# Kernel optimization log

Hardware: AMD Instinct MI355X
Metric: run time of the kernel (lower is better)

Reference implementation:

```python
import jax, jax.numpy as jnp
import numpy as np

N = 20000; E = 320000; IN = 512; H = 4; C = 128; HC = H * C; SD = 2; SE = 128
NEG = 0.01      # nn.LeakyReLU default slope (post-norm activations)
ATT_NEG = 0.2   # GATv2 attention LeakyReLU slope


def _gatv2(x, wl, bl, wr, br, att, bias, src, dst, concat):
    # PyG GATv2Conv (eval mode, add_self_loops already applied to src/dst)
    n = x.shape[0]
    xl = (x @ wl.T + bl).reshape(n, H, C)   # source-side projection
    xr = (x @ wr.T + br).reshape(n, H, C)   # target-side projection
    e = jax.nn.leaky_relu(xl[src] + xr[dst], ATT_NEG)        # [Etot, H, C]
    logits = jnp.einsum('ehc,hc->eh', e, att)                # [Etot, H]
    m = jax.ops.segment_max(logits, dst, num_segments=n)     # segment softmax over dst
    ez = jnp.exp(logits - m[dst])
    denom = jax.ops.segment_sum(ez, dst, num_segments=n)
    alpha = ez / denom[dst]
    out = jax.ops.segment_sum(xl[src] * alpha[:, :, None], dst, num_segments=n)  # [n, H, C]
    out = out.reshape(n, HC) if concat else out.mean(axis=1)
    return out + bias, alpha


def _bn(x, g, b):
    # BatchNorm1d, training-mode batch statistics (biased variance), eps=1e-5
    mu = x.mean(0)
    v = x.var(0)
    return g * (x - mu) * jax.lax.rsqrt(v + 1e-5) + b


def setup_inputs() -> dict:
    key = jax.random.key(0)
    ks = jax.random.split(key, 20)
    p = lambda i, shape: jax.random.normal(ks[i], shape, jnp.float32) * 0.05
    return dict(
        x=jax.random.normal(ks[0], (N, IN), jnp.float32),
        edge_index=jax.random.randint(ks[1], (2, E), 0, N),
        spatial_coords=jax.random.uniform(ks[2], (N, SD), dtype=jnp.float32),
        w1_l=p(3, (HC, IN)), b1_l=jnp.zeros((HC,)), w1_r=p(4, (HC, IN)), b1_r=jnp.zeros((HC,)),
        att1=p(5, (H, C)), bias1=jnp.zeros((HC,)), bn1_g=jnp.ones((HC,)), bn1_b=jnp.zeros((HC,)),
        w2_l=p(6, (HC, HC)), b2_l=jnp.zeros((HC,)), w2_r=p(7, (HC, HC)), b2_r=jnp.zeros((HC,)),
        att2=p(8, (H, C)), bias2=jnp.zeros((HC,)), bn2_g=jnp.ones((HC,)), bn2_b=jnp.zeros((HC,)),
        w3_l=p(9, (HC, HC)), b3_l=jnp.zeros((HC,)), w3_r=p(10, (HC, HC)), b3_r=jnp.zeros((HC,)),
        att3=p(11, (H, C)), bias3=jnp.zeros((C,)), bn3_g=jnp.ones((C,)), bn3_b=jnp.zeros((C,)),
        sp_w1=p(12, (SE, SD)), sp_b1=jnp.zeros((SE,)),
        sp_w2=p(13, (C, SE)), sp_b2=jnp.zeros((C,)),
        mha_in_w=p(14, (3 * SE, SE)), mha_in_b=jnp.zeros((3 * SE,)),
        mha_out_w=p(15, (SE, SE)), mha_out_b=jnp.zeros((SE,)),
        gate_w=p(16, (1, 2 * C)), gate_b=jnp.zeros((1,)),
    )


def reference(x, edge_index, spatial_coords,
              w1_l, b1_l, w1_r, b1_r, att1, bias1, bn1_g, bn1_b,
              w2_l, b2_l, w2_r, b2_r, att2, bias2, bn2_g, bn2_b,
              w3_l, b3_l, w3_r, b3_r, att3, bias3, bn3_g, bn3_b,
              sp_w1, sp_b1, sp_w2, sp_b2,
              mha_in_w, mha_in_b, mha_out_w, mha_out_b,
              gate_w, gate_b):
    loop = jnp.arange(N)
    src = jnp.concatenate([edge_index[0], loop])  # add self loops (PyG default)
    dst = jnp.concatenate([edge_index[1], loop])

    h1, a1 = _gatv2(x, w1_l, b1_l, w1_r, b1_r, att1, bias1, src, dst, True)
    h1 = jax.nn.leaky_relu(_bn(h1, bn1_g, bn1_b), NEG)
    h2, a2 = _gatv2(h1, w2_l, b2_l, w2_r, b2_r, att2, bias2, src, dst, True)
    h2 = jax.nn.leaky_relu(_bn(h2, bn2_g, bn2_b), NEG)
    z, a3 = _gatv2(h2, w3_l, b3_l, w3_r, b3_r, att3, bias3, src, dst, False)
    z = jax.nn.leaky_relu(_bn(z, bn3_g, bn3_b), NEG)

    # spatial embedding MLP (Linear -> LeakyReLU -> Linear -> LeakyReLU)
    emb = jax.nn.leaky_relu(spatial_coords @ sp_w1.T + sp_b1, NEG)
    emb = jax.nn.leaky_relu(emb @ sp_w2.T + sp_b2, NEG)
    # MultiheadAttention over a length-1 sequence: softmax over a single key is 1,
    # so output = W_o (W_v e + b_v) + b_o
    wv = mha_in_w[2 * SE:]
    bv = mha_in_b[2 * SE:]
    sp = (emb @ wv.T + bv) @ mha_out_w.T + mha_out_b  # [N, C]

    gate = jax.nn.softmax(jnp.concatenate([z, sp], axis=-1) @ gate_w.T + gate_b, axis=-1)  # [N,1] (all ones: size-1 softmax, faithful to source)
    z = gate * z + (1.0 - gate) * sp
    return z, a1, a2, a3, gate
```

## Files before the change

### kernel.cpp

```cpp
#include <hip/hip_runtime.h>
#include <math.h>

#define NN 20000
#define EE 320000
#define ETOT 340000
#define DEGCAP 128

typedef __attribute__((ext_vector_type(8))) short short8;
typedef __attribute__((ext_vector_type(4))) float f32x4;

__device__ __forceinline__ float lrelu(float x, float s) { return fmaxf(x, s * x); }
__device__ __forceinline__ float bf2f(ushort u) {
    union { uint i; float f; } c;
    c.i = ((uint)u) << 16;
    return c.f;
}
__device__ __forceinline__ ushort f2bf(float f) {
    uint u = __float_as_uint(f);
    uint r = (u + 0x7FFFu + ((u >> 16) & 1u)) >> 16;
    return (ushort)r;
}
__device__ __forceinline__ void gload16(const ushort* g, const ushort* l) {
    __builtin_amdgcn_global_load_lds((const __attribute__((address_space(1))) void*)g,
                                     (__attribute__((address_space(3))) void*)l, 16, 0, 0);
}

__global__ __launch_bounds__(1024) void k_scan(const int* __restrict__ counts, int* __restrict__ rstart) {
    __shared__ int sm[1024];
    int t = threadIdx.x;
    const int CH = 20;
    int base = t * CH;
    int loc[CH];
    int s = 0;
#pragma unroll
    for (int j = 0; j < CH; ++j) {
        int idx = base + j;
        int v = (idx < NN) ? counts[idx] : 0;
        loc[j] = s;
        s += v;
    }
    sm[t] = s;
    __syncthreads();
    for (int o = 1; o < 1024; o <<= 1) {
        int v = (t >= o) ? sm[t - o] : 0;
        __syncthreads();
        if (t >= o) sm[t] += v;
        __syncthreads();
    }
    int off = sm[t] - s;
#pragma unroll
    for (int j = 0; j < CH; ++j) {
        int idx = base + j;
        if (idx < NN) rstart[idx] = off + loc[j];
    }
    if (t == 1023) rstart[NN] = sm[1023];
}

__global__ void k_scatter(const int* __restrict__ ei, const int* __restrict__ rstart,
                          int* __restrict__ cursor, int* __restrict__ csr) {
    int i = blockIdx.x * blockDim.x + threadIdx.x;
    if (i >= ETOT) return;
    int d = (i < EE) ? ei[EE + i] : (i - EE);
    int pos = atomicAdd(&cursor[d], 1);
    csr[rstart[d] + pos] = i;
}

__global__ void k_prep(const float* __restrict__ x, const float* __restrict__ w0, const float* __restrict__ w1,
                       const float* __restrict__ w2, const float* __restrict__ w3, const float* __restrict__ w4,
                       const float* __restrict__ w5, ushort* __restrict__ xout, ushort* __restrict__ wout,
                       const int* __restrict__ ei, int* __restrict__ counts) {
    int b = blockIdx.x, t = threadIdx.x;
    if (b < 10000) {
        int i = (b * 256 + t) * 4;
        float4 v = *(const float4*)(x + i);
        uint2 pk;
        pk.x = (uint)f2bf(v.x) | ((uint)f2bf(v.y) << 16);
        pk.y = (uint)f2bf(v.z) | ((uint)f2bf(v.w) << 16);
        *(uint2*)(xout + i) = pk;
    } else if (b < 11536) {
        int q = (b - 10000) * 256 + t;
        if (q >= 6 * 65536) return;
        int which = q >> 16;
        int off = (q & 65535) << 2;
        const float* src = which == 0 ? w0 : which == 1 ? w1 : which == 2 ? w2 : which == 3 ? w3 : which == 4 ? w4 : w5;
        float4 v = *(const float4*)(src + off);
        uint2 pk;
        pk.x = (uint)f2bf(v.x) | ((uint)f2bf(v.y) << 16);
        pk.y = (uint)f2bf(v.z) | ((uint)f2bf(v.w) << 16);
        *(uint2*)(wout + which * 262144 + off) = pk;
    } else {
        int i = (b - 11536) * 256 + t;
        if (i >= ETOT) return;
        int d = (i < EE) ? ei[EE + i] : (i - EE);
        atomicAdd(&counts[d], 1);
    }
}

__global__ __launch_bounds__(256) void k_gemm2(const ushort* __restrict__ A, const ushort* __restrict__ W,
                                               const float* __restrict__ bl, const float* __restrict__ br,
                                               ushort* __restrict__ XL, ushort* __restrict__ XR) {
    __shared__ ushort As[8][128][8];
    __shared__ ushort Bs[8][128][8];
    int tid = threadIdx.x;
    int wid = tid >> 6, lane = tid & 63;
    int wm = wid >> 1, wn = wid & 1;
    int bid = blockIdx.x;
    int L = (bid & 7) * 157 + (bid >> 3);
    int mt = L >> 3, nt = L & 7;
    int bm = mt * 128, bn = nt * 128;
    const float* bias = (nt >= 4) ? br : bl;
    ushort* C = (nt >= 4) ? XR : XL;
    int cb = bn - ((nt >= 4) ? 512 : 0);
    int lrow = lane & 15, lslot = lane >> 4;
    const ushort* gA[4];
    const ushort* gB[4];
    const ushort* lA[4];
    const ushort* lB[4];
    const ushort* flatA = &As[0][0][0];
    const ushort* flatB = &Bs[0][0][0];
#pragma unroll
    for (int q = 0; q < 4; ++q) {
        int cbch = wid * 64 + 256 * q;
        lA[q] = flatA + (size_t)cbch * 8;
        lB[q] = flatB + (size_t)cbch * 8;
        int c = cbch + lane;
        int r = c & 127, ks = c >> 7;
        int ar = bm + r;
        if (ar >= NN) ar = NN - 1;
        gA[q] = A + (size_t)ar * 512 + ks * 8;
        gB[q] = W + (size_t)(bn + r) * 512 + ks * 8;
    }
    f32x4 acc[4][4] = {};
    for (int k0 = 0; k0 < 512; k0 += 64) {
#pragma unroll
        for (int q = 0; q < 4; ++q) {
            gload16(gA[q] + k0, lA[q]);
            gload16(gB[q] + k0, lB[q]);
        }
        __syncthreads();
#pragma unroll
        for (int ks = 0; ks < 2; ++ks) {
            short8 af[4], bfr[4];
#pragma unroll
            for (int i = 0; i < 4; ++i) af[i] = *(const short8*)&As[ks * 4 + lslot][wm * 64 + i * 16 + lrow][0];
#pragma unroll
            for (int j = 0; j < 4; ++j) bfr[j] = *(const short8*)&Bs[ks * 4 + lslot][wn * 64 + j * 16 + lrow][0];
#pragma unroll
            for (int i = 0; i < 4; ++i)
#pragma unroll
                for (int j = 0; j < 4; ++j)
                    acc[i][j] = __builtin_amdgcn_mfma_f32_16x16x32_bf16(af[i], bfr[j], acc[i][j], 0, 0, 0);
        }
        __syncthreads();
    }
#pragma unroll
    for (int i = 0; i < 4; ++i) {
#pragma unroll
        for (int j = 0; j < 4; ++j) {
            int gcol = cb + wn * 64 + j * 16 + lrow;
            float bv = bias[gcol];
            int growb = bm + wm * 64 + i * 16 + lslot * 4;
#pragma unroll
            for (int reg = 0; reg < 4; ++reg) {
                int grow = growb + reg;
                if (grow < NN) C[(size_t)grow * 512 + gcol] = f2bf(acc[i][j][reg] + bv);
            }
        }
    }
}

__global__ __launch_bounds__(256) void k_fused(const ushort* __restrict__ xl, const ushort* __restrict__ xr,
                                               const float* __restrict__ att, const int* __restrict__ ei,
                                               const int* __restrict__ rstart, const int* __restrict__ csr,
                                               const float* __restrict__ bias, float* __restrict__ alpha,
                                               ushort* __restrict__ dest, float* __restrict__ bzero, int meanHeads) {
    __shared__ float slg[4][DEGCAP][4];
    __shared__ int ssrc[4][DEGCAP];
    if (blockIdx.x == 0) {
        float4 z = {0.f, 0.f, 0.f, 0.f};
        ((float4*)bzero)[threadIdx.x] = z;
    }
    int w = threadIdx.x >> 6, lane = threadIdx.x & 63;
    int node = blockIdx.x * 4 + w;
    int s0 = rstart[node];
    int deg = rstart[node + 1] - s0;
    int hh = lane >> 4;
    short8 xrv = *(const short8*)(xr + (size_t)node * 512 + lane * 8);
    const float4* at = (const float4*)att + lane * 2;
    float4 a0 = at[0], a1 = at[1];
    float attv[8] = {a0.x, a0.y, a0.z, a0.w, a1.x, a1.y, a1.z, a1.w};
    float xrf[8];
#pragma unroll
    for (int j = 0; j < 8; ++j) xrf[j] = bf2f((ushort)xrv[j]);
    for (int i = lane; i < deg; i += 64) {
        int e = csr[s0 + i];
        ssrc[w][i < DEGCAP ? i : 0] = (e < EE) ? ei[e] : e - EE;
    }
    float m = -1e30f, denom = 0.f;
    float acc[8] = {};
    int scur = ssrc[w][0];
    short8 row = *(const short8*)(xl + (size_t)scur * 512 + lane * 8);
    for (int i = 0; i < deg; ++i) {
        short8 rown = row;
        if (i + 1 < deg) {
            int sn = ssrc[w][(i + 1) < DEGCAP ? (i + 1) : 0];
            rown = *(const short8*)(xl + (size_t)sn * 512 + lane * 8);
        }
        float rf[8];
#pragma unroll
        for (int j = 0; j < 8; ++j) rf[j] = bf2f((ushort)row[j]);
        float p = 0.f;
#pragma unroll
        for (int j = 0; j < 8; ++j) {
            float e = rf[j] + xrf[j];
            p = fmaf(fmaxf(e, 0.2f * e), attv[j], p);
        }
        p += __shfl_xor(p, 1);
        p += __shfl_xor(p, 2);
        p += __shfl_xor(p, 4);
        p += __shfl_xor(p, 8);
        if ((lane & 15) == 0 && i < DEGCAP) slg[w][i][hh] = p;
        if (p <= m) {
            float wg = __expf(p - m);
            denom += wg;
#pragma unroll
            for (int j = 0; j < 8; ++j) acc[j] = fmaf(wg, rf[j], acc[j]);
        } else {
            float sc = __expf(m - p);
            denom = fmaf(denom, sc, 1.f);
#pragma unroll
            for (int j = 0; j < 8; ++j) acc[j] = fmaf(acc[j], sc, rf[j]);
            m = p;
        }
        row = rown;
    }
    float rd = 1.f / denom;
    float m0 = __shfl(m, 0), m1 = __shfl(m, 16), m2 = __shfl(m, 32), m3 = __shfl(m, 48);
    float r0 = __shfl(rd, 0), r1 = __shfl(rd, 16), r2 = __shfl(rd, 32), r3 = __shfl(rd, 48);
    int nal = deg < DEGCAP ? deg : DEGCAP;
    for (int i = lane; i < nal; i += 64) {
        int e = csr[s0 + i];
        float4 l = *(const float4*)&slg[w][i][0];
        float4 av;
        av.x = __expf(l.x - m0) * r0;
        av.y = __expf(l.y - m1) * r1;
        av.z = __expf(l.z - m2) * r2;
        av.w = __expf(l.w - m3) * r3;
        *(float4*)(alpha + (size_t)e * 4) = av;
    }
#pragma unroll
    for (int j = 0; j < 8; ++j) acc[j] *= rd;
    if (!meanHeads) {
        int c = lane * 8;
        short8 o;
#pragma unroll
        for (int j = 0; j < 8; ++j) o[j] = (short)f2bf(acc[j] + bias[c + j]);
        *(short8*)(dest + (size_t)node * 512 + c) = o;
    } else {
#pragma unroll
        for (int j = 0; j < 8; ++j) {
            acc[j] += __shfl_xor(acc[j], 16);
            acc[j] += __shfl_xor(acc[j], 32);
        }
        if (lane < 16) {
            int c = lane * 8;
            short8 o;
#pragma unroll
            for (int j = 0; j < 8; ++j) o[j] = (short)f2bf(0.25f * acc[j] + bias[c + j]);
            *(short8*)(dest + (size_t)node * 128 + c) = o;
        }
    }
}

__global__ void k_bnstats(const ushort* __restrict__ X, float* __restrict__ s, float* __restrict__ s2, int npairs) {
    int t = threadIdx.x;
    if (t >= npairs) return;
    float a0 = 0.f, a1 = 0.f, q0 = 0.f, q1 = 0.f;
    for (int r = blockIdx.x; r < NN; r += gridDim.x) {
        uint p = ((const uint*)X)[r * npairs + t];
        float v0 = bf2f((ushort)(p & 0xffffu));
        float v1 = bf2f((ushort)(p >> 16));
        a0 += v0; q0 += v0 * v0;
        a1 += v1; q1 += v1 * v1;
    }
    atomicAdd(&s[2 * t], a0);
    atomicAdd(&s[2 * t + 1], a1);
    atomicAdd(&s2[2 * t], q0);
    atomicAdd(&s2[2 * t + 1], q1);
}

__global__ void k_bnapply(const ushort* __restrict__ X, const float* __restrict__ g, const float* __restrict__ b,
                          const float* __restrict__ bsum, const float* __restrict__ bsq, float* __restrict__ Yf,
                          ushort* __restrict__ Yb, float* __restrict__ gout, int mask4, int n4) {
    int i = blockIdx.x * blockDim.x + threadIdx.x;
    if (gout && i < NN) gout[i] = 1.0f;
    if (i >= n4) return;
    int c = (i & mask4) << 2;
    uint2 p = ((const uint2*)X)[i];
    float x0 = bf2f((ushort)(p.x & 0xffffu)), x1 = bf2f((ushort)(p.x >> 16));
    float x2 = bf2f((ushort)(p.y & 0xffffu)), x3 = bf2f((ushort)(p.y >> 16));
    float4 S = *(const float4*)(bsum + c);
    float4 Q = *(const float4*)(bsq + c);
    float4 G = *(const float4*)(g + c);
    float4 B = *(const float4*)(b + c);
    const float inv = 1.f / NN;
    float mx = S.x * inv, my = S.y * inv, mz = S.z * inv, mw = S.w * inv;
    float rx = rsqrtf(Q.x * inv - mx * mx + 1e-5f);
    float ry = rsqrtf(Q.y * inv - my * my + 1e-5f);
    float rz = rsqrtf(Q.z * inv - mz * mz + 1e-5f);
    float rw = rsqrtf(Q.w * inv - mw * mw + 1e-5f);
    float4 y;
    y.x = lrelu(G.x * (x0 - mx) * rx + B.x, 0.01f);
    y.y = lrelu(G.y * (x1 - my) * ry + B.y, 0.01f);
    y.z = lrelu(G.z * (x2 - mz) * rz + B.z, 0.01f);
    y.w = lrelu(G.w * (x3 - mw) * rw + B.w, 0.01f);
    if (Yb) {
        uint2 pk;
        pk.x = (uint)f2bf(y.x) | ((uint)f2bf(y.y) << 16);
        pk.y = (uint)f2bf(y.z) | ((uint)f2bf(y.w) << 16);
        *(uint2*)(Yb + (size_t)i * 4) = pk;
    } else {
        ((float4*)Yf)[i] = y;
    }
}

extern "C" void kernel_launch(void* const* d_in, const int* in_sizes, int n_in,
                              void* d_out, int out_size, void* d_ws, size_t ws_size,
                              hipStream_t stream) {
    const float* x = (const float*)d_in[0];
    const int* ei = (const int*)d_in[1];
    const float* wl[3] = {(const float*)d_in[3], (const float*)d_in[11], (const float*)d_in[19]};
    const float* bl[3] = {(const float*)d_in[4], (const float*)d_in[12], (const float*)d_in[20]};
    const float* wr[3] = {(const float*)d_in[5], (const float*)d_in[13], (const float*)d_in[21]};
    const float* br[3] = {(const float*)d_in[6], (const float*)d_in[14], (const float*)d_in[22]};
    const float* att[3] = {(const float*)d_in[7], (const float*)d_in[15], (const float*)d_in[23]};
    const float* bias[3] = {(const float*)d_in[8], (const float*)d_in[16], (const float*)d_in[24]};
    const float* bng[3] = {(const float*)d_in[9], (const float*)d_in[17], (const float*)d_in[25]};
    const float* bnb[3] = {(const float*)d_in[10], (const float*)d_in[18], (const float*)d_in[26]};

    ushort* a_bf = (ushort*)d_ws;
    ushort* xl_bf = a_bf + (size_t)NN * 512;
    ushort* xr_bf = xl_bf + (size_t)NN * 512;
    ushort* h_bf = xr_bf + (size_t)NN * 512;
    ushort* wbuf = h_bf + (size_t)NN * 512;
    float* fp = (float*)(wbuf + 6 * 262144);
    float* bsum = fp;
    float* bsq = bsum + 512;
    int* counts = (int*)(bsq + 512);
    int* cursor = counts + NN;
    int* rstart = cursor + NN;
    int* csr = rstart + (NN + 1);
    size_t need = (size_t)((char*)(csr + ETOT) - (char*)d_ws);
    if (ws_size < need) return;

    float* out = (float*)d_out;
    float* zout = out;
    float* aout[3] = {out + 2560000, out + 3920000, out + 5280000};
    float* gout = out + 6640000;

    hipMemsetAsync(counts, 0, 2 * NN * sizeof(int), stream);
    k_prep<<<12865, 256, 0, stream>>>(x, wl[0], wr[0], wl[1], wr[1], wl[2], wr[2], a_bf, wbuf, ei, counts);
    k_scan<<<1, 1024, 0, stream>>>(counts, rstart);
    k_scatter<<<(ETOT + 255) / 256, 256, 0, stream>>>(ei, rstart, cursor, csr);

    for (int l = 0; l < 3; ++l) {
        const ushort* wb = wbuf + (size_t)l * 524288;
        k_gemm2<<<1256, 256, 0, stream>>>(a_bf, wb, bl[l], br[l], xl_bf, xr_bf);
        int ncols = (l == 2) ? 128 : 512;
        k_fused<<<NN / 4, 256, 0, stream>>>(xl_bf, xr_bf, att[l], ei, rstart, csr, bias[l], aout[l], h_bf,
                                            bsum, (l == 2) ? 1 : 0);
        k_bnstats<<<240, 256, 0, stream>>>(h_bf, bsum, bsq, ncols / 2);
        int n4 = NN * ncols / 4;
        if (l < 2) {
            k_bnapply<<<(n4 + 255) / 256, 256, 0, stream>>>(h_bf, bng[l], bnb[l], bsum, bsq, nullptr, a_bf,
                                                            nullptr, ncols / 4 - 1, n4);
        } else {
            k_bnapply<<<(n4 + 255) / 256, 256, 0, stream>>>(h_bf, bng[l], bnb[l], bsum, bsq, zout, nullptr,
                                                            gout, ncols / 4 - 1, n4);
        }
    }
}
```

Measured before the change: 696.3 us.

## Use 512-thread GEMM blocks with 8 warps and smaller K-step

The projection GEMM now runs 8 wavefronts per 128x128 tile (2x4 warp grid, each 64x32) instead of 4, and the K-loop steps by 32 instead of 64 with half-size LDS buffers. Each thread issues one async global-to-LDS load per operand per step. The aim is more latency hiding through more waves and lower per-thread register pressure. The cost is twice as many barriers per tile and less MFMA work between syncs.

Result: faster. 655.1 us (-5.9%).

```diff
diff --git a/kernel.cpp b/kernel.cpp
--- a/kernel.cpp
+++ b/kernel.cpp
@@ -96,14 +96,14 @@
     }
 }
 
-__global__ __launch_bounds__(256) void k_gemm2(const ushort* __restrict__ A, const ushort* __restrict__ W,
-                                               const float* __restrict__ bl, const float* __restrict__ br,
-                                               ushort* __restrict__ XL, ushort* __restrict__ XR) {
-    __shared__ ushort As[8][128][8];
-    __shared__ ushort Bs[8][128][8];
+__global__ __launch_bounds__(512, 4) void k_gemm2(const ushort* __restrict__ A, const ushort* __restrict__ W,
+                                                  const float* __restrict__ bl, const float* __restrict__ br,
+                                                  ushort* __restrict__ XL, ushort* __restrict__ XR) {
+    __shared__ ushort As[4][128][8];
+    __shared__ ushort Bs[4][128][8];
     int tid = threadIdx.x;
     int wid = tid >> 6, lane = tid & 63;
-    int wm = wid >> 1, wn = wid & 1;
+    int wm = wid >> 2, wn = wid & 3;
     int bid = blockIdx.x;
     int L = (bid & 7) * 157 + (bid >> 3);
     int mt = L >> 3, nt = L & 7;
@@ -112,52 +112,35 @@
     ushort* C = (nt >= 4) ? XR : XL;
     int cb = bn - ((nt >= 4) ? 512 : 0);
     int lrow = lane & 15, lslot = lane >> 4;
-    const ushort* gA[4];
-    const ushort* gB[4];
-    const ushort* lA[4];
-    const ushort* lB[4];
-    const ushort* flatA = &As[0][0][0];
-    const ushort* flatB = &Bs[0][0][0];
-#pragma unroll
-    for (int q = 0; q < 4; ++q) {
-        int cbch = wid * 64 + 256 * q;
-        lA[q] = flatA + (size_t)cbch * 8;
-        lB[q] = flatB + (size_t)cbch * 8;
-        int c = cbch + lane;
-        int r = c & 127, ks = c >> 7;
-        int ar = bm + r;
-        if (ar >= NN) ar = NN - 1;
-        gA[q] = A + (size_t)ar * 512 + ks * 8;
-        gB[q] = W + (size_t)(bn + r) * 512 + ks * 8;
-    }
-    f32x4 acc[4][4] = {};
-    for (int k0 = 0; k0 < 512; k0 += 64) {
-#pragma unroll
-        for (int q = 0; q < 4; ++q) {
-            gload16(gA[q] + k0, lA[q]);
-            gload16(gB[q] + k0, lB[q]);
-        }
+    int r = tid & 127, ks = tid >> 7;
+    int ar = bm + r;
+    if (ar >= NN) ar = NN - 1;
+    const ushort* gA = A + (size_t)ar * 512 + ks * 8;
+    const ushort* gB = W + (size_t)(bn + r) * 512 + ks * 8;
+    const ushort* lA = &As[0][0][0] + (size_t)(wid * 64) * 8;
+    const ushort* lB = &Bs[0][0][0] + (size_t)(wid * 64) * 8;
+    f32x4 acc[4][2] = {};
+    for (int k0 = 0; k0 < 512; k0 += 32) {
+        gload16(gA + k0, lA);
+        gload16(gB + k0, lB);
         __syncthreads();
-#pragma unroll
-        for (int ks = 0; ks < 2; ++ks) {
-            short8 af[4], bfr[4];
-#pragma unroll
-            for (int i = 0; i < 4; ++i) af[i] = *(const short8*)&As[ks * 4 + lslot][wm * 64 + i * 16 + lrow][0];
-#pragma unroll
-            for (int j = 0; j < 4; ++j) bfr[j] = *(const short8*)&Bs[ks * 4 + lslot][wn * 64 + j * 16 + lrow][0];
-#pragma unroll
-            for (int i = 0; i < 4; ++i)
-#pragma unroll
-                for (int j = 0; j < 4; ++j)
-                    acc[i][j] = __builtin_amdgcn_mfma_f32_16x16x32_bf16(af[i], bfr[j], acc[i][j], 0, 0, 0);
-        }
+        short8 af[4], bfr[2];
+#pragma unroll
+        for (int i = 0; i < 4; ++i) af[i] = *(const short8*)&As[lslot][wm * 64 + i * 16 + lrow][0];
+#pragma unroll
+        for (int j = 0; j < 2; ++j) bfr[j] = *(const short8*)&Bs[lslot][wn * 32 + j * 16 + lrow][0];
+#pragma unroll
+        for (int i = 0; i < 4; ++i)
+#pragma unroll
+            for (int j = 0; j < 2; ++j)
+                acc[i][j] = __builtin_amdgcn_mfma_f32_16x16x32_bf16(af[i], bfr[j], acc[i][j], 0, 0, 0);
         __syncthreads();
     }
 #pragma unroll
     for (int i = 0; i < 4; ++i) {
 #pragma unroll
-        for (int j = 0; j < 4; ++j) {
-            int gcol = cb + wn * 64 + j * 16 + lrow;
+        for (int j = 0; j < 2; ++j) {
+            int gcol = cb + wn * 32 + j * 16 + lrow;
             float bv = bias[gcol];
             int growb = bm + wm * 64 + i * 16 + lslot * 4;
 #pragma unroll
@@ -365,7 +348,7 @@
 
     for (int l = 0; l < 3; ++l) {
         const ushort* wb = wbuf + (size_t)l * 524288;
-        k_gemm2<<<1256, 256, 0, stream>>>(a_bf, wb, bl[l], br[l], xl_bf, xr_bf);
+        k_gemm2<<<1256, 512, 0, stream>>>(a_bf, wb, bl[l], br[l], xl_bf, xr_bf);
         int ncols = (l == 2) ? 128 : 512;
         k_fused<<<NN / 4, 256, 0, stream>>>(xl_bf, xr_bf, att[l], ei, rstart, csr, bias[l], aout[l], h_bf,
                                             bsum, (l == 2) ? 1 : 0);
```
